# Optimization experiments

Hardware: AMD Instinct MI355X
Metric: run time of the kernel (lower is better)

## Reference

```python
import jax, jax.numpy as jnp
import numpy as np


def setup_inputs() -> dict:
    key = jax.random.key(0)
    k1, k2, k3 = jax.random.split(key, 3)
    T, B, D, H = 256, 64, 1024, 2048
    sigma = 0.01
    inputs = jax.random.normal(k1, (T, B, D), dtype=jnp.float32)
    state = jnp.zeros((B, H), dtype=jnp.float32)
    W_xh = jax.random.uniform(k2, (D, H), dtype=jnp.float32) * sigma
    W_hh = jax.random.uniform(k3, (H, H), dtype=jnp.float32) * sigma
    b_h = jnp.zeros((H,), dtype=jnp.float32)
    return {"inputs": inputs, "state": state, "W_xh": W_xh, "W_hh": W_hh, "b_h": b_h}


def reference(inputs, state, W_xh, W_hh, b_h):
    # Precompute input projection for all steps in one big GEMM: [T,B,H]
    x_proj = jnp.einsum('tbd,dh->tbh', inputs, W_xh) + b_h

    def step(h, xp):
        h = jnp.tanh(h @ W_hh + xp)
        return h, h

    final_state, outputs = jax.lax.scan(step, state, x_proj)
    # outputs: [T, B, H] (stacked per-step hidden states), final_state: [B, H]
    return outputs, final_state
```

## Files before the change

### kernel.cpp

```cpp
#include <hip/hip_runtime.h>
#include <hip/hip_bf16.h>

#define T_STEPS 256
#define B_SZ    64
#define D_SZ    1024
#define H_SZ    2048
#define NBLK    256
#define TPB     320
#define HBUF    (B_SZ * H_SZ)

#define W_SCALE     256.0f
#define W_INV_SCALE 0.00390625f

#define SENT_ULL 0x7FFF7FFF7FFF7FFFull

typedef __attribute__((ext_vector_type(8))) _Float16 f16x8;
typedef __attribute__((ext_vector_type(4))) _Float16 f16x4;
typedef __attribute__((ext_vector_type(4))) float    f32x4;

#define PREP_NI   16384
#define PREP_NTX  (64 * 32)
#define PREP_NTH  (64 * 64)
#define PREP_NS   128
#define PREP_NC   1
#define PREP_NF   16384
#define PREP_TOT  (PREP_NI + PREP_NTX + PREP_NTH + PREP_NS + PREP_NC + PREP_NF)

__device__ __forceinline__ void tile_transpose(
    const float* __restrict__ in, _Float16* __restrict__ out,
    int rows, int cols, int bx, int by, float scale, float (*tile)[33]) {
    int tx = threadIdx.x & 31, ty = threadIdx.x >> 5;
    int r0 = by * 32, c0 = bx * 32;
#pragma unroll
    for (int i = 0; i < 32; i += 8)
        tile[ty + i][tx] = in[(size_t)(r0 + ty + i) * cols + c0 + tx];
    __syncthreads();
#pragma unroll
    for (int i = 0; i < 32; i += 8)
        out[(size_t)(c0 + ty + i) * rows + r0 + tx] = (_Float16)(tile[tx][ty + i] * scale);
}

__global__ void prep_all(const float* __restrict__ inputs, _Float16* __restrict__ xin,
                         const float* __restrict__ W_xh, _Float16* __restrict__ WxT,
                         const float* __restrict__ W_hh, _Float16* __restrict__ WhT,
                         const float* __restrict__ state, _Float16* __restrict__ h0,
                         unsigned int* __restrict__ ctr, uint4* __restrict__ sfill) {
    __shared__ float tile[32][33];
    int bid = blockIdx.x, tid = threadIdx.x;
    if (bid < PREP_NI) {
        int i = bid * 256 + tid;
        float4 v = ((const float4*)inputs)[i];
        f16x4 o = { (_Float16)v.x, (_Float16)v.y, (_Float16)v.z, (_Float16)v.w };
        ((f16x4*)xin)[i] = o;
    } else if (bid < PREP_NI + PREP_NTX) {
        int rel = bid - PREP_NI;
        tile_transpose(W_xh, WxT, D_SZ, H_SZ, rel % 64, rel / 64, W_SCALE, tile);
    } else if (bid < PREP_NI + PREP_NTX + PREP_NTH) {
        int rel = bid - PREP_NI - PREP_NTX;
        tile_transpose(W_hh, WhT, H_SZ, H_SZ, rel % 64, rel / 64, W_SCALE, tile);
    } else if (bid < PREP_NI + PREP_NTX + PREP_NTH + PREP_NS) {
        int rel = bid - PREP_NI - PREP_NTX - PREP_NTH;
        int i = rel * 256 + tid;
        float4 v = ((const float4*)state)[i];
        f16x4 o = { (_Float16)v.x, (_Float16)v.y, (_Float16)v.z, (_Float16)v.w };
        ((f16x4*)h0)[i] = o;
    } else if (bid < PREP_NI + PREP_NTX + PREP_NTH + PREP_NS + PREP_NC) {
#pragma unroll
        for (int k = 0; k < 4; k++) ctr[k * 256 + tid] = 0u;
    } else if (sfill) {
        int rel = bid - (PREP_NI + PREP_NTX + PREP_NTH + PREP_NS + PREP_NC);
        uint4 s = { 0x7FFF7FFFu, 0x7FFF7FFFu, 0x7FFF7FFFu, 0x7FFF7FFFu };
        sfill[(size_t)rel * 256 + tid] = s;
    }
}

#define GBK 32
__device__ __forceinline__ void gload_lds16(const _Float16* g, _Float16* l) {
    __builtin_amdgcn_global_load_lds((const __attribute__((address_space(1))) void*)g,
                                     (__attribute__((address_space(3))) void*)l, 16, 0, 0);
}

__global__ __launch_bounds__(256) void gemm_xproj(
    const _Float16* __restrict__ A,
    const _Float16* __restrict__ BT,
    const float* __restrict__ bias,
    float* __restrict__ C,
    int M, int N, int K)
{
    __shared__ _Float16 As[128 * GBK];
    __shared__ _Float16 Bs[128 * GBK];

    int tid  = threadIdx.x;
    int wave = tid >> 6;
    int lane = tid & 63;
    int q = lane >> 4;
    int r = lane & 15;
    int m0 = blockIdx.x * 128;
    int n0 = blockIdx.y * 128;
    int wr = (wave >> 1) * 64;
    int wc = (wave & 1) * 64;

    int srow  = lane >> 2;
    int skoff = (lane & 3) * 8;

    f32x4 acc[4][4] = {};
    for (int k0 = 0; k0 < K; k0 += GBK) {
#pragma unroll
        for (int i = 0; i < 2; i++) {
            int chunk = wave * 2 + i;
            int row = chunk * 16 + srow;
            gload_lds16(A  + (size_t)(m0 + row) * K + k0 + skoff, As + chunk * 512);
            gload_lds16(BT + (size_t)(n0 + row) * K + k0 + skoff, Bs + chunk * 512);
        }
        __asm__ volatile("s_waitcnt vmcnt(0)" ::: "memory");
        __syncthreads();

        f16x8 a[4], b[4];
#pragma unroll
        for (int i = 0; i < 4; i++)
            a[i] = *(const f16x8*)(As + (wr + i * 16 + r) * GBK + q * 8);
#pragma unroll
        for (int j = 0; j < 4; j++)
            b[j] = *(const f16x8*)(Bs + (wc + j * 16 + r) * GBK + q * 8);
#pragma unroll
        for (int i = 0; i < 4; i++)
#pragma unroll
            for (int j = 0; j < 4; j++)
                acc[i][j] = __builtin_amdgcn_mfma_f32_16x16x32_f16(a[i], b[j], acc[i][j], 0, 0, 0);
        __syncthreads();
    }
#pragma unroll
    for (int i = 0; i < 4; i++)
#pragma unroll
        for (int j = 0; j < 4; j++)
#pragma unroll
            for (int reg = 0; reg < 4; reg++) {
                int row = m0 + wr + i * 16 + q * 4 + reg;
                int col = n0 + wc + j * 16 + r;
                C[(size_t)row * N + col] = acc[i][j][reg] * W_INV_SCALE + bias[col];
            }
}

template<bool CHAIN>
__global__ __launch_bounds__(TPB, 1) void rnn_persist(
    _Float16* __restrict__ hbase,
    _Float16* __restrict__ hb1,
    const _Float16* __restrict__ WT,
    float* __restrict__ out,
    float* __restrict__ final_out,
    unsigned int* __restrict__ ctr)
{
    __shared__ f16x8 wfrag[8192];
    __shared__ float part[4][2][256];
    __shared__ __align__(16) _Float16 hsl[16 * 32];
    __shared__ int pdone[4];
    __shared__ int hdone1, go;

    int tid = threadIdx.x;
    int bid = blockIdx.x;
    int g   = (bid >> 1) & 3;
    int c   = ((bid >> 3) << 1) | (bid & 1);
    int n0  = c * 32;
    int row0 = g * 16;

    if (tid == 0) {
        pdone[0] = pdone[1] = pdone[2] = pdone[3] = 0;
        hdone1 = 0; go = 0;
    }

    for (int idx = tid; idx < 8192; idx += TPB) {
        int kb = idx >> 7, j = (idx >> 6) & 1, l = idx & 63;
        wfrag[idx] = *(const f16x8*)(WT + (size_t)(n0 + j * 16 + (l & 15)) * H_SZ
                                        + kb * 32 + (l >> 4) * 8);
    }
    __syncthreads();

    int wave = tid >> 6, lane = tid & 63;

    if (wave == 4) {
        float c0 = 1.0f + lane, c1 = 2.0f, c2 = 3.0f, c3 = 4.0f;
        const float k1 = 1.0000001f, k2 = 1.0e-30f;
        while (__hip_atomic_load(&go, __ATOMIC_RELAXED, __HIP_MEMORY_SCOPE_WORKGROUP) < T_STEPS) {
#pragma unroll
            for (int z = 0; z < 64; z++) {
                c0 = __builtin_fmaf(c0, k1, k2);
                c1 = __builtin_fmaf(c1, k1, k2);
                c2 = __builtin_fmaf(c2, k1, k2);
                c3 = __builtin_fmaf(c3, k1, k2);
            }
        }
        __asm__ volatile("" :: "v"(c0), "v"(c1), "v"(c2), "v"(c3));
        return;
    }

    int q = lane >> 4, r = lane & 15;
    unsigned int* aline = ctr + (g * 2 + (bid & 1)) * 32;

    float xp[4];
    if (wave < 2) {
#pragma unroll
        for (int s = 0; s < 4; s++)
            xp[s] = out[(size_t)(row0 + q + 4 * s) * H_SZ + n0 + wave * 16 + r];
    }

    union AU { unsigned long long u[2]; f16x8 v; };

    for (int t = 0; t < T_STEPS; t++) {
        const _Float16* hp;
        _Float16*       hn;
        if constexpr (CHAIN) {
            hp = hbase + (size_t)t * HBUF;
            hn = hbase + (size_t)(t + 1) * HBUF;
        } else {
            hp = (t & 1) ? hb1 : hbase;
            hn = (t & 1) ? hbase : hb1;
        }
        float* out_t = out + (size_t)t * B_SZ * H_SZ;
        int tg = t + 1;

        const _Float16* arow = hp + (size_t)(row0 + r) * H_SZ + q * 8;
        AU ab[16];
        if constexpr (CHAIN) {
#pragma unroll
            for (int p = 0; p < 16; p++)
                ab[p].v = *(const f16x8*)(arow + (wave * 16 + p) * 32);
            bool bad = false;
#pragma unroll
            for (int p = 0; p < 16; p++)
                bad = bad | (ab[p].u[0] == SENT_ULL) | (ab[p].u[1] == SENT_ULL);
            if (t > 0 && __ballot(bad) != 0ull) {
                const unsigned long long* abase = (const unsigned long long*)arow;
                for (;;) {
#pragma unroll
                    for (int p = 0; p < 16; p++) {
                        const unsigned long long* a = abase + (size_t)(wave * 16 + p) * 8;
                        ab[p].u[0] = __hip_atomic_load(a,     __ATOMIC_RELAXED, __HIP_MEMORY_SCOPE_AGENT);
                        ab[p].u[1] = __hip_atomic_load(a + 1, __ATOMIC_RELAXED, __HIP_MEMORY_SCOPE_AGENT);
                    }
                    bool b2 = false;
#pragma unroll
                    for (int p = 0; p < 16; p++)
                        b2 = b2 | (ab[p].u[0] == SENT_ULL) | (ab[p].u[1] == SENT_ULL);
                    if (__ballot(b2) == 0ull) break;
                    __builtin_amdgcn_s_sleep(1);
                }
            }
            __asm__ volatile("" ::: "memory");
        } else {
#pragma unroll
            for (int p = 0; p < 16; p++) {
                ab[p].u[0] = __hip_atomic_load((unsigned long long*)(arow + (wave * 16 + p) * 32),
                                               __ATOMIC_RELAXED, __HIP_MEMORY_SCOPE_AGENT);
                ab[p].u[1] = __hip_atomic_load((unsigned long long*)(arow + (wave * 16 + p) * 32) + 1,
                                               __ATOMIC_RELAXED, __HIP_MEMORY_SCOPE_AGENT);
            }
        }

        f32x4 acc[2] = {};
#pragma unroll
        for (int p = 0; p < 16; p++) {
            int kb = wave * 16 + p;
            acc[0] = __builtin_amdgcn_mfma_f32_16x16x32_f16(ab[p].v, wfrag[kb * 128 + lane],      acc[0], 0, 0, 0);
            acc[1] = __builtin_amdgcn_mfma_f32_16x16x32_f16(ab[p].v, wfrag[kb * 128 + 64 + lane], acc[1], 0, 0, 0);
        }

#pragma unroll
        for (int h = 0; h < 2; h++)
            *(f32x4*)&part[wave][h][lane * 4] = acc[h];
        __asm__ volatile("s_waitcnt lgkmcnt(0)" ::: "memory");
        if (lane == 0)
            __hip_atomic_store(&pdone[wave], tg, __ATOMIC_RELAXED, __HIP_MEMORY_SCOPE_WORKGROUP);

        if (wave >= 2) {
            if (t == T_STEPS - 1) break;
            while (__hip_atomic_load(&go, __ATOMIC_RELAXED, __HIP_MEMORY_SCOPE_WORKGROUP) < tg) { }
            continue;
        }

        for (int w = 0; w < 4; w++)
            if (w != wave)
                while (__hip_atomic_load(&pdone[w], __ATOMIC_RELAXED, __HIP_MEMORY_SCOPE_WORKGROUP) < tg) { }
        __asm__ volatile("" ::: "memory");

        bool last = (t == T_STEPS - 1);
        float vv[4];
#pragma unroll
        for (int s = 0; s < 4; s++) {
            int idx = (s * 16 + r) * 4 + q;
            float sum = part[0][wave][idx] + part[1][wave][idx]
                      + part[2][wave][idx] + part[3][wave][idx];
            vv[s] = tanhf(sum * W_INV_SCALE + xp[s]);
            hsl[(q + 4 * s) * 32 + wave * 16 + r] = (_Float16)vv[s];
        }

        if (!last) {
            __asm__ volatile("s_waitcnt lgkmcnt(0)" ::: "memory");
            int rl = lane >> 2, pi = wave * 4 + (lane & 3);
            unsigned long long hv = ((const unsigned long long*)hsl)[rl * 8 + pi];
            __hip_atomic_store((unsigned long long*)(hn + (size_t)(row0 + rl) * H_SZ + n0) + pi,
                               hv, __ATOMIC_RELAXED, __HIP_MEMORY_SCOPE_AGENT);
        }

#pragma unroll
        for (int s = 0; s < 4; s++) {
            size_t o = (size_t)(row0 + q + 4 * s) * H_SZ + n0 + wave * 16 + r;
            out_t[o] = vv[s];
            if (last) final_out[o] = vv[s];
        }
        if (last) {
            if (wave == 0 && lane == 0)
                __hip_atomic_store(&go, T_STEPS, __ATOMIC_RELAXED, __HIP_MEMORY_SCOPE_WORKGROUP);
            break;
        }

        const float* out_t1 = out_t + B_SZ * H_SZ;
#pragma unroll
        for (int s = 0; s < 4; s++)
            xp[s] = out_t1[(size_t)(row0 + q + 4 * s) * H_SZ + n0 + wave * 16 + r];

        if (wave == 1) {
            if (lane == 0)
                __hip_atomic_store(&hdone1, tg, __ATOMIC_RELAXED, __HIP_MEMORY_SCOPE_WORKGROUP);
            while (__hip_atomic_load(&go, __ATOMIC_RELAXED, __HIP_MEMORY_SCOPE_WORKGROUP) < tg) { }
            continue;
        }
        while (__hip_atomic_load(&hdone1, __ATOMIC_RELAXED, __HIP_MEMORY_SCOPE_WORKGROUP) < tg) { }
        if (lane == 0)
            __hip_atomic_fetch_add(aline, 1u, __ATOMIC_RELAXED, __HIP_MEMORY_SCOPE_AGENT);
        unsigned int line_tgt = (unsigned int)tg * 32u;
        for (;;) {
            unsigned int v = __hip_atomic_load(ctr + (g * 2 + (lane & 1)) * 32,
                                               __ATOMIC_RELAXED, __HIP_MEMORY_SCOPE_AGENT);
            if (__ballot(v < line_tgt) == 0ull) break;
        }
        if (lane == 0)
            __hip_atomic_store(&go, tg, __ATOMIC_RELAXED, __HIP_MEMORY_SCOPE_WORKGROUP);
    }
}


extern "C" void kernel_launch(void* const* d_in, const int* in_sizes, int n_in,
                              void* d_out, int out_size, void* d_ws, size_t ws_size,
                              hipStream_t stream) {
    const float* inputs = (const float*)d_in[0];
    const float* state  = (const float*)d_in[1];
    const float* W_xh   = (const float*)d_in[2];
    const float* W_hh   = (const float*)d_in[3];
    const float* b_h    = (const float*)d_in[4];
    float* out = (float*)d_out;
    char* ws = (char*)d_ws;

    const size_t MB = 1ull << 20;
    const size_t XIN_BYTES = (size_t)T_STEPS * B_SZ * D_SZ * 2;

    const size_t OFF_WXT   = 0;
    const size_t OFF_WHT   = 4 * MB;
    const size_t OFF_CTR   = 12 * MB;
    const size_t OFF_XIN   = 12 * MB + 8192;
    const size_t OFF_CHAIN = OFF_XIN + XIN_BYTES;
    const size_t NEED_CHAIN = OFF_CHAIN + (size_t)(T_STEPS + 1) * HBUF * 2;

    const size_t F_IN  = 0;
    const size_t F_WXT = F_IN  + XIN_BYTES;
    const size_t F_WHT = F_WXT + (size_t)H_SZ * D_SZ * 2;
    const size_t F_H0  = F_WHT + (size_t)H_SZ * H_SZ * 2;
    const size_t F_H1  = F_H0  + (size_t)HBUF * 2;
    const size_t F_CTR = F_H1  + (size_t)HBUF * 2;
    const size_t NEED_PP = F_CTR + 4096;

    dim3 g1((T_STEPS * B_SZ) / 128, H_SZ / 128);
    float* final_out = out + (size_t)T_STEPS * B_SZ * H_SZ;

    if (ws_size >= NEED_CHAIN) {
        _Float16* WxT    = (_Float16*)(ws + OFF_WXT);
        _Float16* WhT    = (_Float16*)(ws + OFF_WHT);
        unsigned int* ctr = (unsigned int*)(ws + OFF_CTR);
        _Float16* xin    = (_Float16*)(ws + OFF_XIN);
        _Float16* hchain = (_Float16*)(ws + OFF_CHAIN);
        _Float16* hb1 = nullptr;

        prep_all<<<PREP_TOT, 256, 0, stream>>>(inputs, xin, W_xh, WxT,
                                               W_hh, WhT, state, hchain, ctr,
                                               (uint4*)(hchain + HBUF));

        gemm_xproj<<<g1, 256, 0, stream>>>(xin, WxT, b_h, out,
                                           T_STEPS * B_SZ, H_SZ, D_SZ);

        void* args[] = { (void*)&hchain, (void*)&hb1, (void*)&WhT,
                         (void*)&out, (void*)&final_out, (void*)&ctr };
        hipLaunchCooperativeKernel((void*)rnn_persist<true>, dim3(NBLK), dim3(TPB),
                                   args, 0, stream);
    } else {
        if (ws_size < NEED_PP) return;
        _Float16* inputs_f16 = (_Float16*)(ws + F_IN);
        _Float16* WxT    = (_Float16*)(ws + F_WXT);
        _Float16* WhT    = (_Float16*)(ws + F_WHT);
        _Float16* hbuf0  = (_Float16*)(ws + F_H0);
        _Float16* hbuf1  = (_Float16*)(ws + F_H1);
        unsigned int* ctr = (unsigned int*)(ws + F_CTR);

        prep_all<<<PREP_TOT, 256, 0, stream>>>(inputs, inputs_f16, W_xh, WxT,
                                               W_hh, WhT, state, hbuf0, ctr,
                                               (uint4*)nullptr);

        gemm_xproj<<<g1, 256, 0, stream>>>(inputs_f16, WxT, b_h, out,
                                           T_STEPS * B_SZ, H_SZ, D_SZ);

        void* args[] = { (void*)&hbuf0, (void*)&hbuf1, (void*)&WhT,
                         (void*)&out, (void*)&final_out, (void*)&ctr };
        hipLaunchCooperativeKernel((void*)rnn_persist<false>, dim3(NBLK), dim3(TPB),
                                   args, 0, stream);
    }
}
```

Measured before the change: 1.500 ms.

## Replace atomic-counter grid barrier with per-wave flag array polled by helper wave

```diff
diff --git a/kernel.cpp b/kernel.cpp
--- a/kernel.cpp
+++ b/kernel.cpp
@@ -154,7 +154,8 @@
     __shared__ float part[4][2][256];
     __shared__ __align__(16) _Float16 hsl[16 * 32];
     __shared__ int pdone[4];
-    __shared__ int hdone1, go;
+    __shared__ int pread[2];
+    __shared__ int go4[4];
 
     int tid = threadIdx.x;
     int bid = blockIdx.x;
@@ -165,7 +166,8 @@
 
     if (tid == 0) {
         pdone[0] = pdone[1] = pdone[2] = pdone[3] = 0;
-        hdone1 = 0; go = 0;
+        pread[0] = pread[1] = 0;
+        go4[0] = go4[1] = go4[2] = go4[3] = 0;
     }
 
     for (int idx = tid; idx < 8192; idx += TPB) {
@@ -176,25 +178,44 @@
     __syncthreads();
 
     int wave = tid >> 6, lane = tid & 63;
+    unsigned int* arr = ctr + g * 128;
 
     if (wave == 4) {
+        const unsigned int* aw = arr + lane * 2;
+        int myset = lane >> 4;
+        bool leader = (lane == (myset << 4));
         float c0 = 1.0f + lane, c1 = 2.0f, c2 = 3.0f, c3 = 4.0f;
         const float k1 = 1.0000001f, k2 = 1.0e-30f;
-        while (__hip_atomic_load(&go, __ATOMIC_RELAXED, __HIP_MEMORY_SCOPE_WORKGROUP) < T_STEPS) {
-#pragma unroll
-            for (int z = 0; z < 64; z++) {
+        for (;;) {
+            unsigned int v0 = __hip_atomic_load(aw,     __ATOMIC_RELAXED, __HIP_MEMORY_SCOPE_AGENT);
+            unsigned int v1 = __hip_atomic_load(aw + 1, __ATOMIC_RELAXED, __HIP_MEMORY_SCOPE_AGENT);
+#pragma unroll
+            for (int z = 0; z < 48; z++) {
                 c0 = __builtin_fmaf(c0, k1, k2);
                 c1 = __builtin_fmaf(c1, k1, k2);
                 c2 = __builtin_fmaf(c2, k1, k2);
                 c3 = __builtin_fmaf(c3, k1, k2);
             }
+            unsigned int m = v0 < v1 ? v0 : v1;
+#pragma unroll
+            for (int k = 1; k <= 8; k <<= 1) {
+                unsigned int o = __shfl_xor(m, k);
+                m = o < m ? o : m;
+            }
+            if (leader)
+                __hip_atomic_store(&go4[myset], (int)m, __ATOMIC_RELAXED, __HIP_MEMORY_SCOPE_WORKGROUP);
+            unsigned int g2 = m;
+            {
+                unsigned int o = __shfl_xor(g2, 16); g2 = o < g2 ? o : g2;
+                o = __shfl_xor(g2, 32);              g2 = o < g2 ? o : g2;
+            }
+            if (g2 >= (unsigned int)(T_STEPS - 1)) break;
         }
         __asm__ volatile("" :: "v"(c0), "v"(c1), "v"(c2), "v"(c3));
         return;
     }
 
     int q = lane >> 4, r = lane & 15;
-    unsigned int* aline = ctr + (g * 2 + (bid & 1)) * 32;
 
     float xp[4];
     if (wave < 2) {
@@ -218,6 +239,11 @@
         float* out_t = out + (size_t)t * B_SZ * H_SZ;
         int tg = t + 1;
 
+        if (t > 0) {
+            while (__hip_atomic_load(&go4[wave], __ATOMIC_RELAXED, __HIP_MEMORY_SCOPE_WORKGROUP) < t) { }
+            __asm__ volatile("" ::: "memory");
+        }
+
         const _Float16* arow = hp + (size_t)(row0 + r) * H_SZ + q * 8;
         AU ab[16];
         if constexpr (CHAIN) {
@@ -264,6 +290,12 @@
             acc[1] = __builtin_amdgcn_mfma_f32_16x16x32_f16(ab[p].v, wfrag[kb * 128 + 64 + lane], acc[1], 0, 0, 0);
         }
 
+        if (t > 0) {
+            while (__hip_atomic_load(&pread[0], __ATOMIC_RELAXED, __HIP_MEMORY_SCOPE_WORKGROUP) < t ||
+                   __hip_atomic_load(&pread[1], __ATOMIC_RELAXED, __HIP_MEMORY_SCOPE_WORKGROUP) < t) { }
+            __asm__ volatile("" ::: "memory");
+        }
+
 #pragma unroll
         for (int h = 0; h < 2; h++)
             *(f32x4*)&part[wave][h][lane * 4] = acc[h];
@@ -273,7 +305,6 @@
 
         if (wave >= 2) {
             if (t == T_STEPS - 1) break;
-            while (__hip_atomic_load(&go, __ATOMIC_RELAXED, __HIP_MEMORY_SCOPE_WORKGROUP) < tg) { }
             continue;
         }
 
@@ -283,13 +314,20 @@
         __asm__ volatile("" ::: "memory");
 
         bool last = (t == T_STEPS - 1);
-        float vv[4];
+        float sums[4];
 #pragma unroll
         for (int s = 0; s < 4; s++) {
             int idx = (s * 16 + r) * 4 + q;
-            float sum = part[0][wave][idx] + part[1][wave][idx]
-                      + part[2][wave][idx] + part[3][wave][idx];
-            vv[s] = tanhf(sum * W_INV_SCALE + xp[s]);
+            sums[s] = part[0][wave][idx] + part[1][wave][idx]
+                    + part[2][wave][idx] + part[3][wave][idx];
+        }
+        if (lane == 0)
+            __hip_atomic_store(&pread[wave], tg, __ATOMIC_RELAXED, __HIP_MEMORY_SCOPE_WORKGROUP);
+
+        float vv[4];
+#pragma unroll
+        for (int s = 0; s < 4; s++) {
+            vv[s] = tanhf(sums[s] * W_INV_SCALE + xp[s]);
             hsl[(q + 4 * s) * 32 + wave * 16 + r] = (_Float16)vv[s];
         }
 
@@ -299,6 +337,11 @@
             unsigned long long hv = ((const unsigned long long*)hsl)[rl * 8 + pi];
             __hip_atomic_store((unsigned long long*)(hn + (size_t)(row0 + rl) * H_SZ + n0) + pi,
                                hv, __ATOMIC_RELAXED, __HIP_MEMORY_SCOPE_AGENT);
+            if constexpr (!CHAIN)
+                __builtin_amdgcn_s_waitcnt(0);
+            if (lane == 0)
+                __hip_atomic_store(arr + c * 2 + wave, (unsigned int)tg,
+                                   __ATOMIC_RELAXED, __HIP_MEMORY_SCOPE_AGENT);
         }
 
 #pragma unroll
@@ -307,34 +350,12 @@
             out_t[o] = vv[s];
             if (last) final_out[o] = vv[s];
         }
-        if (last) {
-            if (wave == 0 && lane == 0)
-                __hip_atomic_store(&go, T_STEPS, __ATOMIC_RELAXED, __HIP_MEMORY_SCOPE_WORKGROUP);
-            break;
-        }
+        if (last) break;
 
         const float* out_t1 = out_t + B_SZ * H_SZ;
 #pragma unroll
         for (int s = 0; s < 4; s++)
             xp[s] = out_t1[(size_t)(row0 + q + 4 * s) * H_SZ + n0 + wave * 16 + r];
-
-        if (wave == 1) {
-            if (lane == 0)
-                __hip_atomic_store(&hdone1, tg, __ATOMIC_RELAXED, __HIP_MEMORY_SCOPE_WORKGROUP);
-            while (__hip_atomic_load(&go, __ATOMIC_RELAXED, __HIP_MEMORY_SCOPE_WORKGROUP) < tg) { }
-            continue;
-        }
-        while (__hip_atomic_load(&hdone1, __ATOMIC_RELAXED, __HIP_MEMORY_SCOPE_WORKGROUP) < tg) { }
-        if (lane == 0)
-            __hip_atomic_fetch_add(aline, 1u, __ATOMIC_RELAXED, __HIP_MEMORY_SCOPE_AGENT);
-        unsigned int line_tgt = (unsigned int)tg * 32u;
-        for (;;) {
-            unsigned int v = __hip_atomic_load(ctr + (g * 2 + (lane & 1)) * 32,
-                                               __ATOMIC_RELAXED, __HIP_MEMORY_SCOPE_AGENT);
-            if (__ballot(v < line_tgt) == 0ull) break;
-        }
-        if (lane == 0)
-            __hip_atomic_store(&go, tg, __ATOMIC_RELAXED, __HIP_MEMORY_SCOPE_WORKGROUP);
     }
 }
 
```

New measurement: 2.599 ms. 73.2% more time.

## Decouple h publication from per-workgroup barrier in sentinel-chained recurrent kernel

Applied to the files above, without the earlier changes.

```diff
diff --git a/kernel.cpp b/kernel.cpp
--- a/kernel.cpp
+++ b/kernel.cpp
@@ -233,9 +233,11 @@
                 for (;;) {
 #pragma unroll
                     for (int p = 0; p < 16; p++) {
-                        const unsigned long long* a = abase + (size_t)(wave * 16 + p) * 8;
-                        ab[p].u[0] = __hip_atomic_load(a,     __ATOMIC_RELAXED, __HIP_MEMORY_SCOPE_AGENT);
-                        ab[p].u[1] = __hip_atomic_load(a + 1, __ATOMIC_RELAXED, __HIP_MEMORY_SCOPE_AGENT);
+                        if (ab[p].u[0] == SENT_ULL || ab[p].u[1] == SENT_ULL) {
+                            const unsigned long long* a = abase + (size_t)(wave * 16 + p) * 8;
+                            ab[p].u[0] = __hip_atomic_load(a,     __ATOMIC_RELAXED, __HIP_MEMORY_SCOPE_AGENT);
+                            ab[p].u[1] = __hip_atomic_load(a + 1, __ATOMIC_RELAXED, __HIP_MEMORY_SCOPE_AGENT);
+                        }
                     }
                     bool b2 = false;
 #pragma unroll
@@ -293,48 +295,93 @@
             hsl[(q + 4 * s) * 32 + wave * 16 + r] = (_Float16)vv[s];
         }
 
-        if (!last) {
+        if constexpr (CHAIN) {
+            if (!last) {
+                __asm__ volatile("s_waitcnt lgkmcnt(0)" ::: "memory");
+                int rl = lane >> 2, pi = wave * 4 + (lane & 3);
+                unsigned long long hv = ((const unsigned long long*)hsl)[rl * 8 + pi];
+                __hip_atomic_store((unsigned long long*)(hn + (size_t)(row0 + rl) * H_SZ + n0) + pi,
+                                   hv, __ATOMIC_RELAXED, __HIP_MEMORY_SCOPE_AGENT);
+                if (lane == 0)
+                    __hip_atomic_fetch_add(aline, 1u, __ATOMIC_RELAXED, __HIP_MEMORY_SCOPE_AGENT);
+            }
+#pragma unroll
+            for (int s = 0; s < 4; s++) {
+                size_t o = (size_t)(row0 + q + 4 * s) * H_SZ + n0 + wave * 16 + r;
+                out_t[o] = vv[s];
+                if (last) final_out[o] = vv[s];
+            }
+            if (last) {
+                if (wave == 0 && lane == 0)
+                    __hip_atomic_store(&go, T_STEPS, __ATOMIC_RELAXED, __HIP_MEMORY_SCOPE_WORKGROUP);
+                break;
+            }
+            const float* out_t1 = out_t + B_SZ * H_SZ;
+#pragma unroll
+            for (int s = 0; s < 4; s++)
+                xp[s] = out_t1[(size_t)(row0 + q + 4 * s) * H_SZ + n0 + wave * 16 + r];
+
+            if (wave == 1) {
+                while (__hip_atomic_load(&go, __ATOMIC_RELAXED, __HIP_MEMORY_SCOPE_WORKGROUP) < tg) { }
+                continue;
+            }
+            unsigned int line_tgt = (unsigned int)tg * 64u;
+            for (;;) {
+                unsigned int v = __hip_atomic_load(ctr + (g * 2 + (lane & 1)) * 32,
+                                                   __ATOMIC_RELAXED, __HIP_MEMORY_SCOPE_AGENT);
+                if (__ballot(v < line_tgt) == 0ull) break;
+            }
+            if (lane == 0)
+                __hip_atomic_store(&go, tg, __ATOMIC_RELAXED, __HIP_MEMORY_SCOPE_WORKGROUP);
+        } else {
+            if (last) {
+                if (wave == 0 && lane == 0)
+                    __hip_atomic_store(&go, T_STEPS, __ATOMIC_RELAXED, __HIP_MEMORY_SCOPE_WORKGROUP);
+#pragma unroll
+                for (int s = 0; s < 4; s++) {
+                    size_t o = (size_t)(row0 + q + 4 * s) * H_SZ + n0 + wave * 16 + r;
+                    out_t[o] = vv[s];
+                    final_out[o] = vv[s];
+                }
+                break;
+            }
+#pragma unroll
+            for (int s = 0; s < 4; s++) {
+                size_t o = (size_t)(row0 + q + 4 * s) * H_SZ + n0 + wave * 16 + r;
+                out_t[o] = vv[s];
+            }
+            const float* out_t1 = out_t + B_SZ * H_SZ;
+#pragma unroll
+            for (int s = 0; s < 4; s++)
+                xp[s] = out_t1[(size_t)(row0 + q + 4 * s) * H_SZ + n0 + wave * 16 + r];
+
             __asm__ volatile("s_waitcnt lgkmcnt(0)" ::: "memory");
-            int rl = lane >> 2, pi = wave * 4 + (lane & 3);
-            unsigned long long hv = ((const unsigned long long*)hsl)[rl * 8 + pi];
-            __hip_atomic_store((unsigned long long*)(hn + (size_t)(row0 + rl) * H_SZ + n0) + pi,
-                               hv, __ATOMIC_RELAXED, __HIP_MEMORY_SCOPE_AGENT);
-        }
-
-#pragma unroll
-        for (int s = 0; s < 4; s++) {
-            size_t o = (size_t)(row0 + q + 4 * s) * H_SZ + n0 + wave * 16 + r;
-            out_t[o] = vv[s];
-            if (last) final_out[o] = vv[s];
-        }
-        if (last) {
-            if (wave == 0 && lane == 0)
-                __hip_atomic_store(&go, T_STEPS, __ATOMIC_RELAXED, __HIP_MEMORY_SCOPE_WORKGROUP);
-            break;
-        }
-
-        const float* out_t1 = out_t + B_SZ * H_SZ;
-#pragma unroll
-        for (int s = 0; s < 4; s++)
-            xp[s] = out_t1[(size_t)(row0 + q + 4 * s) * H_SZ + n0 + wave * 16 + r];
-
-        if (wave == 1) {
+            {
+                int rl = lane >> 2, pi = wave * 4 + (lane & 3);
+                unsigned long long hv = ((const unsigned long long*)hsl)[rl * 8 + pi];
+                __hip_atomic_store((unsigned long long*)(hn + (size_t)(row0 + rl) * H_SZ + n0) + pi,
+                                   hv, __ATOMIC_RELAXED, __HIP_MEMORY_SCOPE_AGENT);
+            }
+            __builtin_amdgcn_s_waitcnt(0);
+
+            if (wave == 1) {
+                if (lane == 0)
+                    __hip_atomic_store(&hdone1, tg, __ATOMIC_RELAXED, __HIP_MEMORY_SCOPE_WORKGROUP);
+                while (__hip_atomic_load(&go, __ATOMIC_RELAXED, __HIP_MEMORY_SCOPE_WORKGROUP) < tg) { }
+                continue;
+            }
+            while (__hip_atomic_load(&hdone1, __ATOMIC_RELAXED, __HIP_MEMORY_SCOPE_WORKGROUP) < tg) { }
             if (lane == 0)
-                __hip_atomic_store(&hdone1, tg, __ATOMIC_RELAXED, __HIP_MEMORY_SCOPE_WORKGROUP);
-            while (__hip_atomic_load(&go, __ATOMIC_RELAXED, __HIP_MEMORY_SCOPE_WORKGROUP) < tg) { }
-            continue;
-        }
-        while (__hip_atomic_load(&hdone1, __ATOMIC_RELAXED, __HIP_MEMORY_SCOPE_WORKGROUP) < tg) { }
-        if (lane == 0)
-            __hip_atomic_fetch_add(aline, 1u, __ATOMIC_RELAXED, __HIP_MEMORY_SCOPE_AGENT);
-        unsigned int line_tgt = (unsigned int)tg * 32u;
-        for (;;) {
-            unsigned int v = __hip_atomic_load(ctr + (g * 2 + (lane & 1)) * 32,
-                                               __ATOMIC_RELAXED, __HIP_MEMORY_SCOPE_AGENT);
-            if (__ballot(v < line_tgt) == 0ull) break;
-        }
-        if (lane == 0)
-            __hip_atomic_store(&go, tg, __ATOMIC_RELAXED, __HIP_MEMORY_SCOPE_WORKGROUP);
+                __hip_atomic_fetch_add(aline, 1u, __ATOMIC_RELAXED, __HIP_MEMORY_SCOPE_AGENT);
+            unsigned int line_tgt = (unsigned int)tg * 32u;
+            for (;;) {
+                unsigned int v = __hip_atomic_load(ctr + (g * 2 + (lane & 1)) * 32,
+                                                   __ATOMIC_RELAXED, __HIP_MEMORY_SCOPE_AGENT);
+                if (__ballot(v < line_tgt) == 0ull) break;
+            }
+            if (lane == 0)
+                __hip_atomic_store(&go, tg, __ATOMIC_RELAXED, __HIP_MEMORY_SCOPE_WORKGROUP);
+        }
     }
 }
 
```

Result: slower. 1.551 ms (+3.4%).
